# Kernel optimization log

Measured on AMD Instinct MI355X. Metric: run time of the kernel, lower is better.

## Reference

```python
import jax, jax.numpy as jnp
import numpy as np

N_NODES = 50000
N_EDGES = 800000
D_IN, D_H, D_E = 512, 512, 256


def setup_inputs() -> dict:
    key = jax.random.key(0)
    ks = jax.random.split(key, 16)

    def lin(kw, kb, fan_in, fan_out):
        s = 1.0 / np.sqrt(fan_in)
        W = jax.random.uniform(kw, (fan_in, fan_out), dtype=jnp.float32, minval=-s, maxval=s)
        b = jax.random.uniform(kb, (fan_out,), dtype=jnp.float32, minval=-s, maxval=s)
        return W, b

    W1, b1 = lin(ks[2], ks[3], D_IN, D_H)
    W2, b2 = lin(ks[4], ks[5], D_H, D_H)
    W3, b3 = lin(ks[6], ks[7], D_H, D_E)
    We, be = lin(ks[8], ks[9], D_E, 7)
    Wh, bh = lin(ks[10], ks[11], D_E, 8)
    Wg, bg = lin(ks[12], ks[13], D_E, 57)

    return {
        "x": jax.random.normal(ks[0], (N_NODES, D_IN), dtype=jnp.float32),
        "edge_index": jax.random.randint(ks[1], (2, N_EDGES), 0, N_NODES, dtype=jnp.int32),
        "W1": W1, "b1": b1, "W2": W2, "b2": b2, "W3": W3, "b3": b3,
        "We": We, "be": be, "Wh": Wh, "bh": bh, "Wg": Wg, "bg": bg,
    }


def reference(x, edge_index, W1, b1, W2, b2, W3, b3, We, be, Wh, bh, Wg, bg):
    n = x.shape[0]
    # GCNConv: add self-loops, symmetric normalization D^{-1/2} A D^{-1/2}
    loops = jnp.arange(n, dtype=edge_index.dtype)
    src = jnp.concatenate([edge_index[0], loops])  # message sources
    dst = jnp.concatenate([edge_index[1], loops])  # aggregation targets
    deg = jax.ops.segment_sum(jnp.ones_like(src, dtype=x.dtype), dst, num_segments=n)
    dis = jnp.where(deg > 0, jax.lax.rsqrt(deg), 0.0)
    norm = (dis[src] * dis[dst])[:, None]  # [E+N, 1]

    def gcn_conv(h, W, b):
        h = h @ W                                   # [n, d_out]
        msg = h[src] * norm                         # gather + scale
        return jax.ops.segment_sum(msg, dst, num_segments=n) + b

    h = jax.nn.relu(gcn_conv(x, W1, b1))
    h = jax.nn.relu(gcn_conv(h, W2, b2))
    emb = gcn_conv(h, W3, b3)
    employment = emb @ We + be
    healthcare = emb @ Wh + bh
    grocery = emb @ Wg + bg
    return emb, employment, healthcare, grocery
```

## Files before the change

### kernel.cpp

```cpp
#include <hip/hip_runtime.h>

#define NN   50000
#define NNP  50048
#define NE   800000
#define DIN  512
#define DH   512
#define DE   256

#define CSR_CAP 1150016

typedef __bf16 bf16_t;
typedef __bf16 bf16x4 __attribute__((ext_vector_type(4)));
typedef __bf16 bf16x8 __attribute__((ext_vector_type(8)));
typedef float  f32x4  __attribute__((ext_vector_type(4)));
typedef _Float16 half_t;
typedef _Float16 half8 __attribute__((ext_vector_type(8)));

#define PB_SPLIT 25024
#define PB_IDEG  3125
#define PB_CSR   1124
#define PB_W1    1024
#define PB_W2    1024
#define PB_W3    512
#define PB_HEADW 80
#define PB_TOTAL (PB_SPLIT + PB_IDEG + PB_CSR + PB_W1 + PB_W2 + PB_W3 + PB_HEADW)

__global__ void k_prep(const float* __restrict__ X, bf16_t* __restrict__ Ah,
                       bf16_t* __restrict__ Al, const int* __restrict__ dst,
                       int* __restrict__ indeg, int* __restrict__ csr,
                       const float* __restrict__ W1, bf16_t* __restrict__ B1h, bf16_t* __restrict__ B1l,
                       const float* __restrict__ W2, bf16_t* __restrict__ B2h, bf16_t* __restrict__ B2l,
                       const float* __restrict__ W3, bf16_t* __restrict__ B3h, bf16_t* __restrict__ B3l,
                       const float* __restrict__ We, const float* __restrict__ be,
                       const float* __restrict__ Wh, const float* __restrict__ bh,
                       const float* __restrict__ Wg, const float* __restrict__ bg,
                       bf16_t* __restrict__ Wth, bf16_t* __restrict__ Wtl,
                       float* __restrict__ bc) {
    int b = blockIdx.x;
    if (b < PB_SPLIT) {
        long idx = (long)b * 256 + threadIdx.x;
        long base = idx * 4;
        int row = (int)(base >> 9);
        f32x4 v;
        if (row < NN) v = *(const f32x4*)(X + base);
        else { v[0] = 0.f; v[1] = 0.f; v[2] = 0.f; v[3] = 0.f; }
        bf16x4 h, l;
        #pragma unroll
        for (int c = 0; c < 4; ++c) {
            float f = v[c];
            bf16_t hh = (bf16_t)f;
            h[c] = hh;
            l[c] = (bf16_t)(f - (float)hh);
        }
        *(bf16x4*)(Ah + base) = h;
        *(bf16x4*)(Al + base) = l;
        return;
    }
    b -= PB_SPLIT;
    if (b < PB_IDEG) {
        int i = b * 256 + threadIdx.x;
        atomicAdd(&indeg[dst[i]], 1);
        return;
    }
    b -= PB_IDEG;
    if (b < PB_CSR) {
        int i = b * 256 + threadIdx.x;
        if (i < CSR_CAP / 4) ((int4*)csr)[i] = make_int4(NN, NN, NN, NN);
        return;
    }
    b -= PB_CSR;
    if (b < PB_W1) {
        int idx = b * 256 + threadIdx.x;
        int k = idx >> 9, n = idx & 511;
        float f = W1[idx];
        bf16_t h = (bf16_t)f;
        B1h[(size_t)n * DIN + k] = h;
        B1l[(size_t)n * DIN + k] = (bf16_t)(f - (float)h);
        return;
    }
    b -= PB_W1;
    if (b < PB_W2) {
        int idx = b * 256 + threadIdx.x;
        int k = idx >> 9, n = idx & 511;
        float f = W2[idx];
        bf16_t h = (bf16_t)f;
        B2h[(size_t)n * DH + k] = h;
        B2l[(size_t)n * DH + k] = (bf16_t)(f - (float)h);
        return;
    }
    b -= PB_W2;
    if (b < PB_W3) {
        int idx = b * 256 + threadIdx.x;
        int k = idx >> 8, n = idx & 255;
        float f = W3[idx];
        bf16_t h = (bf16_t)f;
        B3h[(size_t)n * DH + k] = h;
        B3l[(size_t)n * DH + k] = (bf16_t)(f - (float)h);
        return;
    }
    b -= PB_W3;
    {
        int idx = b * 256 + threadIdx.x;
        int n = idx / 256, k = idx % 256;
        float f = 0.f;
        if (n < 7)       f = We[k * 7 + n];
        else if (n < 15) f = Wh[k * 8 + (n - 7)];
        else if (n < 72) f = Wg[k * 57 + (n - 15)];
        bf16_t h = (bf16_t)f;
        Wth[idx] = h;
        Wtl[idx] = (bf16_t)(f - (float)h);
        if (k == 0) {
            float bb = 0.f;
            if (n < 7)       bb = be[n];
            else if (n < 15) bb = bh[n - 7];
            else if (n < 72) bb = bg[n - 15];
            bc[n] = bb;
        }
    }
}

#define SCAN_BLOCKS 49

__global__ __launch_bounds__(1024) void k_scan_a(const int* __restrict__ indeg,
                                                 int* __restrict__ rowptr,
                                                 float* __restrict__ dis,
                                                 int* __restrict__ bsum) {
    __shared__ int wsum[16];
    const int tid = threadIdx.x, lane = tid & 63, wid = tid >> 6;
    const int i = blockIdx.x * 1024 + tid;
    int deg = (i < NN) ? indeg[i] : 0;
    int v = (deg + 7) & ~7;
    int x = v;
    #pragma unroll
    for (int d = 1; d < 64; d <<= 1) {
        int t = __shfl_up(x, d, 64);
        if (lane >= d) x += t;
    }
    if (lane == 63) wsum[wid] = x;
    __syncthreads();
    if (wid == 0) {
        int s = (lane < 16) ? wsum[lane] : 0;
        #pragma unroll
        for (int d = 1; d < 16; d <<= 1) {
            int t = __shfl_up(s, d, 64);
            if (lane >= d) s += t;
        }
        if (lane < 16) wsum[lane] = s;
    }
    __syncthreads();
    int woff = (wid > 0) ? wsum[wid - 1] : 0;
    if (i < NN) {
        rowptr[i] = x - v + woff;
        dis[i] = rsqrtf((float)(deg + 1));
    }
    if (tid == 0) bsum[blockIdx.x] = wsum[15];
}

__global__ __launch_bounds__(64) void k_scan_b(const int* __restrict__ bsum,
                                               int* __restrict__ boff,
                                               int* __restrict__ rowptr,
                                               float* __restrict__ dis) {
    const int lane = threadIdx.x;
    int v = (lane < SCAN_BLOCKS) ? bsum[lane] : 0;
    int x = v;
    #pragma unroll
    for (int d = 1; d < 64; d <<= 1) {
        int t = __shfl_up(x, d, 64);
        if (lane >= d) x += t;
    }
    if (lane < SCAN_BLOCKS) boff[lane] = x - v;
    if (lane == SCAN_BLOCKS - 1) rowptr[NN] = x;
    if (lane == 0) dis[NN] = 0.f;
}

__global__ void k_scan_c(const int* __restrict__ boff, int* __restrict__ rowptr,
                         int* __restrict__ cursor) {
    int i = blockIdx.x * blockDim.x + threadIdx.x;
    if (i < NN) {
        int r = rowptr[i] + boff[i >> 10];
        rowptr[i] = r;
        cursor[i] = r;
    }
}

__global__ void k_fill(const int* __restrict__ src, const int* __restrict__ dst,
                       int* __restrict__ cursor, int* __restrict__ csr, int e) {
    int i = blockIdx.x * blockDim.x + threadIdx.x;
    if (i < e) {
        int d = dst[i];
        int p = atomicAdd(&cursor[d], 1);
        csr[p] = src[i];
    }
}


__device__ __forceinline__ void gld_lds16(const void* g, void* l) {
    __builtin_amdgcn_global_load_lds(
        (const __attribute__((address_space(1))) unsigned int*)g,
        (__attribute__((address_space(3))) unsigned int*)l, 16, 0, 0);
}

__global__ __launch_bounds__(256) void k_gemm_split(
    const bf16_t* __restrict__ Ah, const bf16_t* __restrict__ Al,
    const bf16_t* __restrict__ Bh, const bf16_t* __restrict__ Bl,
    half_t* __restrict__ C, int M, int N, int K) {
    __shared__ alignas(16) bf16_t sAh[128 * 32];
    __shared__ alignas(16) bf16_t sAl[128 * 32];
    __shared__ alignas(16) bf16_t sBh[128 * 32];
    __shared__ alignas(16) bf16_t sBl[128 * 32];

    const int tid = threadIdx.x;
    const int wave = tid >> 6, lane = tid & 63;
    const int quad = lane >> 4, l16 = lane & 15;
    const int bm = blockIdx.y * 128, bn = blockIdx.x * 128;
    const int wm = (wave & 1) * 64, wn = (wave >> 1) * 64;

    f32x4 acc[4][4];
    #pragma unroll
    for (int i = 0; i < 4; ++i)
        #pragma unroll
        for (int j = 0; j < 4; ++j)
            #pragma unroll
            for (int r = 0; r < 4; ++r) acc[i][j][r] = 0.f;

    const int srow = wave * 32 + (lane >> 2);
    const int sseg = (lane & 3) * 16;
    char* lds0A = (char*)sAh + wave * 32 * 64;
    char* lds0a = (char*)sAl + wave * 32 * 64;
    char* lds0B = (char*)sBh + wave * 32 * 64;
    char* lds0b = (char*)sBl + wave * 32 * 64;

    const char* gAh0 = (const char*)(Ah + (size_t)(bm + srow) * K) + sseg;
    const char* gAl0 = (const char*)(Al + (size_t)(bm + srow) * K) + sseg;
    const char* gBh0 = (const char*)(Bh + (size_t)(bn + srow) * K) + sseg;
    const char* gBl0 = (const char*)(Bl + (size_t)(bn + srow) * K) + sseg;
    const size_t rstep = (size_t)16 * K * 2;

    for (int k0 = 0; k0 < K; k0 += 32) {
        const size_t kb = (size_t)k0 * 2;
        gld_lds16(gAh0 + kb,         lds0A);
        gld_lds16(gAh0 + kb + rstep, lds0A + 1024);
        gld_lds16(gAl0 + kb,         lds0a);
        gld_lds16(gAl0 + kb + rstep, lds0a + 1024);
        gld_lds16(gBh0 + kb,         lds0B);
        gld_lds16(gBh0 + kb + rstep, lds0B + 1024);
        gld_lds16(gBl0 + kb,         lds0b);
        gld_lds16(gBl0 + kb + rstep, lds0b + 1024);
        __syncthreads();

        bf16x8 fah[4], fal[4], fbh[4], fbl[4];
        #pragma unroll
        for (int i = 0; i < 4; ++i) {
            fah[i] = *(const bf16x8*)(sAh + (wm + 16 * i + l16) * 32 + quad * 8);
            fal[i] = *(const bf16x8*)(sAl + (wm + 16 * i + l16) * 32 + quad * 8);
            fbh[i] = *(const bf16x8*)(sBh + (wn + 16 * i + l16) * 32 + quad * 8);
            fbl[i] = *(const bf16x8*)(sBl + (wn + 16 * i + l16) * 32 + quad * 8);
        }
        #pragma unroll
        for (int i = 0; i < 4; ++i)
            #pragma unroll
            for (int j = 0; j < 4; ++j) {
                acc[i][j] = __builtin_amdgcn_mfma_f32_16x16x32_bf16(fah[i], fbh[j], acc[i][j], 0, 0, 0);
                acc[i][j] = __builtin_amdgcn_mfma_f32_16x16x32_bf16(fah[i], fbl[j], acc[i][j], 0, 0, 0);
                acc[i][j] = __builtin_amdgcn_mfma_f32_16x16x32_bf16(fal[i], fbh[j], acc[i][j], 0, 0, 0);
            }
        __syncthreads();
    }

    #pragma unroll
    for (int i = 0; i < 4; ++i) {
        #pragma unroll
        for (int j = 0; j < 4; ++j) {
            int col = bn + wn + 16 * j + l16;
            #pragma unroll
            for (int r = 0; r < 4; ++r) {
                int row = bm + wm + 16 * i + quad * 4 + r;
                if (row < M) C[(size_t)row * N + col] = (half_t)acc[i][j][r];
            }
        }
    }
}


__global__ __launch_bounds__(128) void k_agg_split(
    const half_t* __restrict__ t, const int* __restrict__ rowptr,
    const int* __restrict__ csr, const float* __restrict__ dis,
    const float* __restrict__ bias,
    bf16_t* __restrict__ Ah, bf16_t* __restrict__ Al) {
    const int node = blockIdx.x * 2 + (threadIdx.x >> 6);
    const int lane = threadIdx.x & 63;
    const int beg = rowptr[node], end = rowptr[node + 1];
    const float din = dis[node];
    const char* tc = (const char*)t;
    const unsigned lb = (unsigned)lane * 16u;

    float a0[8], a1[8], a2[8], a3[8];
    #pragma unroll
    for (int c = 0; c < 8; ++c) { a0[c] = 0.f; a1[c] = 0.f; a2[c] = 0.f; a3[c] = 0.f; }

    if (beg < end) {
        int4 sa = *(const int4*)(csr + beg);
        int4 sb = *(const int4*)(csr + beg + 4);
        float w0 = dis[sa.x], w1 = dis[sa.y], w2 = dis[sa.z], w3 = dis[sa.w];
        float w4 = dis[sb.x], w5 = dis[sb.y], w6 = dis[sb.z], w7 = dis[sb.w];
        half8 v0 = *(const half8*)(tc + (((unsigned)sa.x) << 10) + lb);
        half8 v1 = *(const half8*)(tc + (((unsigned)sa.y) << 10) + lb);
        half8 v2 = *(const half8*)(tc + (((unsigned)sa.z) << 10) + lb);
        half8 v3 = *(const half8*)(tc + (((unsigned)sa.w) << 10) + lb);
        half8 v4 = *(const half8*)(tc + (((unsigned)sb.x) << 10) + lb);
        half8 v5 = *(const half8*)(tc + (((unsigned)sb.y) << 10) + lb);
        half8 v6 = *(const half8*)(tc + (((unsigned)sb.z) << 10) + lb);
        half8 v7 = *(const half8*)(tc + (((unsigned)sb.w) << 10) + lb);
        int4 na = sa, nb = sb;
        if (beg + 8 < end) {
            na = *(const int4*)(csr + beg + 8);
            nb = *(const int4*)(csr + beg + 12);
        }
        for (int e = beg; e < end; ) {
            half8 u0 = v0, u1 = v1, u2 = v2, u3 = v3, u4 = v4, u5 = v5, u6 = v6, u7 = v7;
            float x0 = w0, x1 = w1, x2 = w2, x3 = w3, x4 = w4, x5 = w5, x6 = w6, x7 = w7;
            e += 8;
            if (e < end) {
                w0 = dis[na.x]; w1 = dis[na.y]; w2 = dis[na.z]; w3 = dis[na.w];
                w4 = dis[nb.x]; w5 = dis[nb.y]; w6 = dis[nb.z]; w7 = dis[nb.w];
                v0 = *(const half8*)(tc + (((unsigned)na.x) << 10) + lb);
                v1 = *(const half8*)(tc + (((unsigned)na.y) << 10) + lb);
                v2 = *(const half8*)(tc + (((unsigned)na.z) << 10) + lb);
                v3 = *(const half8*)(tc + (((unsigned)na.w) << 10) + lb);
                v4 = *(const half8*)(tc + (((unsigned)nb.x) << 10) + lb);
                v5 = *(const half8*)(tc + (((unsigned)nb.y) << 10) + lb);
                v6 = *(const half8*)(tc + (((unsigned)nb.z) << 10) + lb);
                v7 = *(const half8*)(tc + (((unsigned)nb.w) << 10) + lb);
                if (e + 8 < end) {
                    na = *(const int4*)(csr + e + 8);
                    nb = *(const int4*)(csr + e + 12);
                }
            }
            #pragma unroll
            for (int c = 0; c < 8; ++c) {
                a0[c] = fmaf((float)u0[c], x0, a0[c]);
                a1[c] = fmaf((float)u1[c], x1, a1[c]);
                a2[c] = fmaf((float)u2[c], x2, a2[c]);
                a3[c] = fmaf((float)u3[c], x3, a3[c]);
                a0[c] = fmaf((float)u4[c], x4, a0[c]);
                a1[c] = fmaf((float)u5[c], x5, a1[c]);
                a2[c] = fmaf((float)u6[c], x6, a2[c]);
                a3[c] = fmaf((float)u7[c], x7, a3[c]);
            }
        }
    }

    half8 sv = ((const half8*)(t + (size_t)node * DH))[lane];
    f32x4 bv0 = ((const f32x4*)bias)[lane * 2];
    f32x4 bv1 = ((const f32x4*)bias)[lane * 2 + 1];
    bf16x8 h, l;
    #pragma unroll
    for (int c = 0; c < 8; ++c) {
        float b = (c < 4) ? bv0[c] : bv1[c - 4];
        float acc = (a0[c] + a1[c]) + (a2[c] + a3[c]);
        float o = fmaf(fmaf((float)sv[c], din, acc), din, b);
        o = fmaxf(o, 0.f);
        bf16_t hh = (bf16_t)o;
        h[c] = hh;
        l[c] = (bf16_t)(o - (float)hh);
    }
    *(bf16x8*)(Ah + (size_t)node * DH + lane * 8) = h;
    *(bf16x8*)(Al + (size_t)node * DH + lane * 8) = l;
}

__global__ __launch_bounds__(128) void k_agg_f32(
    const half_t* __restrict__ t, const int* __restrict__ rowptr,
    const int* __restrict__ csr, const float* __restrict__ dis,
    const float* __restrict__ bias, float* __restrict__ out,
    bf16_t* __restrict__ Eh, bf16_t* __restrict__ El) {
    const int node = blockIdx.x * 4 + (threadIdx.x >> 5);
    const int lane = threadIdx.x & 31;
    const int beg = rowptr[node], end = rowptr[node + 1];
    const float din = dis[node];
    const char* tc = (const char*)t;
    const unsigned lb = (unsigned)lane * 16u;

    float a0[8], a1[8], a2[8], a3[8];
    #pragma unroll
    for (int c = 0; c < 8; ++c) { a0[c] = 0.f; a1[c] = 0.f; a2[c] = 0.f; a3[c] = 0.f; }

    if (beg < end) {
        int4 sa = *(const int4*)(csr + beg);
        int4 sb = *(const int4*)(csr + beg + 4);
        float w0 = dis[sa.x], w1 = dis[sa.y], w2 = dis[sa.z], w3 = dis[sa.w];
        float w4 = dis[sb.x], w5 = dis[sb.y], w6 = dis[sb.z], w7 = dis[sb.w];
        half8 v0 = *(const half8*)(tc + (((unsigned)sa.x) << 9) + lb);
        half8 v1 = *(const half8*)(tc + (((unsigned)sa.y) << 9) + lb);
        half8 v2 = *(const half8*)(tc + (((unsigned)sa.z) << 9) + lb);
        half8 v3 = *(const half8*)(tc + (((unsigned)sa.w) << 9) + lb);
        half8 v4 = *(const half8*)(tc + (((unsigned)sb.x) << 9) + lb);
        half8 v5 = *(const half8*)(tc + (((unsigned)sb.y) << 9) + lb);
        half8 v6 = *(const half8*)(tc + (((unsigned)sb.z) << 9) + lb);
        half8 v7 = *(const half8*)(tc + (((unsigned)sb.w) << 9) + lb);
        int4 na = sa, nb = sb;
        if (beg + 8 < end) {
            na = *(const int4*)(csr + beg + 8);
            nb = *(const int4*)(csr + beg + 12);
        }
        for (int e = beg; e < end; ) {
            half8 u0 = v0, u1 = v1, u2 = v2, u3 = v3, u4 = v4, u5 = v5, u6 = v6, u7 = v7;
            float x0 = w0, x1 = w1, x2 = w2, x3 = w3, x4 = w4, x5 = w5, x6 = w6, x7 = w7;
            e += 8;
            if (e < end) {
                w0 = dis[na.x]; w1 = dis[na.y]; w2 = dis[na.z]; w3 = dis[na.w];
                w4 = dis[nb.x]; w5 = dis[nb.y]; w6 = dis[nb.z]; w7 = dis[nb.w];
                v0 = *(const half8*)(tc + (((unsigned)na.x) << 9) + lb);
                v1 = *(const half8*)(tc + (((unsigned)na.y) << 9) + lb);
                v2 = *(const half8*)(tc + (((unsigned)na.z) << 9) + lb);
                v3 = *(const half8*)(tc + (((unsigned)na.w) << 9) + lb);
                v4 = *(const half8*)(tc + (((unsigned)nb.x) << 9) + lb);
                v5 = *(const half8*)(tc + (((unsigned)nb.y) << 9) + lb);
                v6 = *(const half8*)(tc + (((unsigned)nb.z) << 9) + lb);
                v7 = *(const half8*)(tc + (((unsigned)nb.w) << 9) + lb);
                if (e + 8 < end) {
                    na = *(const int4*)(csr + e + 8);
                    nb = *(const int4*)(csr + e + 12);
                }
            }
            #pragma unroll
            for (int c = 0; c < 8; ++c) {
                a0[c] = fmaf((float)u0[c], x0, a0[c]);
                a1[c] = fmaf((float)u1[c], x1, a1[c]);
                a2[c] = fmaf((float)u2[c], x2, a2[c]);
                a3[c] = fmaf((float)u3[c], x3, a3[c]);
                a0[c] = fmaf((float)u4[c], x4, a0[c]);
                a1[c] = fmaf((float)u5[c], x5, a1[c]);
                a2[c] = fmaf((float)u6[c], x6, a2[c]);
                a3[c] = fmaf((float)u7[c], x7, a3[c]);
            }
        }
    }

    half8 sv = ((const half8*)(t + (size_t)node * DE))[lane];
    f32x4 bv0 = ((const f32x4*)bias)[lane * 2];
    f32x4 bv1 = ((const f32x4*)bias)[lane * 2 + 1];
    f32x4 o0, o1;
    bf16x8 hh, ll;
    #pragma unroll
    for (int c = 0; c < 8; ++c) {
        float b = (c < 4) ? bv0[c] : bv1[c - 4];
        float acc = (a0[c] + a1[c]) + (a2[c] + a3[c]);
        float o = fmaf(fmaf((float)sv[c], din, acc), din, b);
        if (c < 4) o0[c] = o; else o1[c - 4] = o;
        bf16_t h = (bf16_t)o;
        hh[c] = h;
        ll[c] = (bf16_t)(o - (float)h);
    }
    ((f32x4*)(out + (size_t)node * DE))[lane * 2]     = o0;
    ((f32x4*)(out + (size_t)node * DE))[lane * 2 + 1] = o1;
    *(bf16x8*)(Eh + (size_t)node * DE + lane * 8) = hh;
    *(bf16x8*)(El + (size_t)node * DE + lane * 8) = ll;
}


__global__ __launch_bounds__(256) void k_heads_mfma(
    const bf16_t* __restrict__ Eh, const bf16_t* __restrict__ El,
    const bf16_t* __restrict__ Wth, const bf16_t* __restrict__ Wtl,
    const float* __restrict__ bc,
    float* __restrict__ oe, float* __restrict__ oh, float* __restrict__ og) {
    const int wave = threadIdx.x >> 6, lane = threadIdx.x & 63;
    const int quad = lane >> 4, l16 = lane & 15;
    const int row0 = blockIdx.x * 64 + wave * 16;

    f32x4 acc[5];
    #pragma unroll
    for (int j = 0; j < 5; ++j)
        #pragma unroll
        for (int r = 0; r < 4; ++r) acc[j][r] = 0.f;

    const size_t abase = (size_t)(row0 + l16) * 256 + quad * 8;
    #pragma unroll
    for (int ks = 0; ks < 256; ks += 32) {
        bf16x8 ah = *(const bf16x8*)(Eh + abase + ks);
        bf16x8 al = *(const bf16x8*)(El + abase + ks);
        #pragma unroll
        for (int j = 0; j < 5; ++j) {
            const size_t bbase = (size_t)(j * 16 + l16) * 256 + ks + quad * 8;
            bf16x8 bh = *(const bf16x8*)(Wth + bbase);
            bf16x8 bl = *(const bf16x8*)(Wtl + bbase);
            acc[j] = __builtin_amdgcn_mfma_f32_16x16x32_bf16(ah, bh, acc[j], 0, 0, 0);
            acc[j] = __builtin_amdgcn_mfma_f32_16x16x32_bf16(ah, bl, acc[j], 0, 0, 0);
            acc[j] = __builtin_amdgcn_mfma_f32_16x16x32_bf16(al, bh, acc[j], 0, 0, 0);
        }
    }

    #pragma unroll
    for (int j = 0; j < 5; ++j) {
        int col = j * 16 + l16;
        if (col < 72) {
            float b = bc[col];
            #pragma unroll
            for (int r = 0; r < 4; ++r) {
                int row = row0 + quad * 4 + r;
                if (row < NN) {
                    float v = acc[j][r] + b;
                    if (col < 7)       oe[(size_t)row * 7 + col] = v;
                    else if (col < 15) oh[(size_t)row * 8 + (col - 7)] = v;
                    else               og[(size_t)row * 57 + (col - 15)] = v;
                }
            }
        }
    }
}


extern "C" void kernel_launch(void* const* d_in, const int* in_sizes, int n_in,
                              void* d_out, int out_size, void* d_ws, size_t ws_size,
                              hipStream_t stream) {
    const float* x   = (const float*)d_in[0];
    const int*   ei  = (const int*)d_in[1];
    const float* W1  = (const float*)d_in[2];
    const float* b1  = (const float*)d_in[3];
    const float* W2  = (const float*)d_in[4];
    const float* b2  = (const float*)d_in[5];
    const float* W3  = (const float*)d_in[6];
    const float* b3  = (const float*)d_in[7];
    const float* We  = (const float*)d_in[8];
    const float* be  = (const float*)d_in[9];
    const float* Wh  = (const float*)d_in[10];
    const float* bh  = (const float*)d_in[11];
    const float* Wg  = (const float*)d_in[12];
    const float* bg  = (const float*)d_in[13];

    const int* e_src = ei;
    const int* e_dst = ei + NE;

    half_t* bufA = (half_t*)d_ws;
    bf16_t* Ah   = (bf16_t*)(bufA + (size_t)NNP * DH);
    bf16_t* Al   = Ah + (size_t)NNP * DH;
    bf16_t* B1h  = Al + (size_t)NNP * DH;
    bf16_t* B1l  = B1h + (size_t)DIN * DH;
    bf16_t* B2h  = B1l + (size_t)DIN * DH;
    bf16_t* B2l  = B2h + (size_t)DH * DH;
    bf16_t* B3h  = B2l + (size_t)DH * DH;
    bf16_t* B3l  = B3h + (size_t)DH * DE;
    bf16_t* embh = B3l + (size_t)DH * DE;
    bf16_t* embl = embh + (size_t)NNP * DE;
    bf16_t* Wth  = embl + (size_t)NNP * DE;
    bf16_t* Wtl  = Wth + 80 * 256;
    float*  bc   = (float*)(Wtl + 80 * 256);
    int*   indeg  = (int*)(bc + 128);
    int*   rowptr = indeg + 50048;
    int*   cursor = rowptr + 50048;
    float* dis    = (float*)(cursor + 50048);
    int*   csr    = (int*)(dis + 50048);
    int*   bsum   = csr + CSR_CAP;
    int*   boff   = bsum + 64;

    float* emb   = (float*)d_out;
    float* out_e = emb + (size_t)NN * DE;
    float* out_h = out_e + (size_t)NN * 7;
    float* out_g = out_h + (size_t)NN * 8;

    hipMemsetAsync(indeg, 0, NN * sizeof(int), stream);
    k_prep<<<PB_TOTAL, 256, 0, stream>>>(x, Ah, Al, e_dst, indeg, csr,
                                         W1, B1h, B1l, W2, B2h, B2l, W3, B3h, B3l,
                                         We, be, Wh, bh, Wg, bg, Wth, Wtl, bc);
    k_scan_a<<<SCAN_BLOCKS, 1024, 0, stream>>>(indeg, rowptr, dis, bsum);
    k_scan_b<<<1, 64, 0, stream>>>(bsum, boff, rowptr, dis);
    k_scan_c<<<(NN + 255) / 256, 256, 0, stream>>>(boff, rowptr, cursor);
    k_fill<<<(NE + 255) / 256, 256, 0, stream>>>(e_src, e_dst, cursor, csr, NE);

    const int gy = NNP / 128;

    k_gemm_split<<<dim3(DH / 128, gy), 256, 0, stream>>>(Ah, Al, B1h, B1l, bufA, NNP, DH, DIN);
    k_agg_split<<<NN / 2, 128, 0, stream>>>(bufA, rowptr, csr, dis, b1, Ah, Al);

    k_gemm_split<<<dim3(DH / 128, gy), 256, 0, stream>>>(Ah, Al, B2h, B2l, bufA, NNP, DH, DH);
    k_agg_split<<<NN / 2, 128, 0, stream>>>(bufA, rowptr, csr, dis, b2, Ah, Al);

    k_gemm_split<<<dim3(DE / 128, gy), 256, 0, stream>>>(Ah, Al, B3h, B3l, bufA, NNP, DE, DH);
    k_agg_f32<<<NN / 4, 128, 0, stream>>>(bufA, rowptr, csr, dis, b3, emb, embh, embl);

    k_heads_mfma<<<NNP / 64, 256, 0, stream>>>(embh, embl, Wth, Wtl, bc, out_e, out_h, out_g);
}
```

Measured before the change: 900.9 us.

## Fold source-degree scaling into GEMM epilogue and use fp16 activations for layers 2-3

Each GEMM epilogue now multiplies its output row by dis[row], so the aggregation kernels no longer gather dis per neighbour and only multiply by the destination's dis. Layers 2 and 3 store activations as a single fp16 array instead of a bf16 hi/lo pair. Their GEMMs use fp16 MFMA with the weights split into an fp16 high part and a residual scaled by 4096, so two MFMA products replace the three-product bf16 split. This cuts activation write and read traffic and the number of MFMAs. The trade is reduced precision, since the activations are no longer split into two parts.

```diff
diff --git a/kernel.cpp b/kernel.cpp
--- a/kernel.cpp
+++ b/kernel.cpp
@@ -25,12 +25,12 @@
 #define PB_HEADW 80
 #define PB_TOTAL (PB_SPLIT + PB_IDEG + PB_CSR + PB_W1 + PB_W2 + PB_W3 + PB_HEADW)
 
-__global__ void k_prep(const float* __restrict__ X, bf16_t* __restrict__ Ah,
-                       bf16_t* __restrict__ Al, const int* __restrict__ dst,
+__global__ void k_prep(const float* __restrict__ X, bf16_t* __restrict__ Xh,
+                       bf16_t* __restrict__ Xl, const int* __restrict__ dst,
                        int* __restrict__ indeg, int* __restrict__ csr,
                        const float* __restrict__ W1, bf16_t* __restrict__ B1h, bf16_t* __restrict__ B1l,
-                       const float* __restrict__ W2, bf16_t* __restrict__ B2h, bf16_t* __restrict__ B2l,
-                       const float* __restrict__ W3, bf16_t* __restrict__ B3h, bf16_t* __restrict__ B3l,
+                       const float* __restrict__ W2, half_t* __restrict__ B2h, half_t* __restrict__ B2l,
+                       const float* __restrict__ W3, half_t* __restrict__ B3h, half_t* __restrict__ B3l,
                        const float* __restrict__ We, const float* __restrict__ be,
                        const float* __restrict__ Wh, const float* __restrict__ bh,
                        const float* __restrict__ Wg, const float* __restrict__ bg,
@@ -52,8 +52,8 @@
             h[c] = hh;
             l[c] = (bf16_t)(f - (float)hh);
         }
-        *(bf16x4*)(Ah + base) = h;
-        *(bf16x4*)(Al + base) = l;
+        *(bf16x4*)(Xh + base) = h;
+        *(bf16x4*)(Xl + base) = l;
         return;
     }
     b -= PB_SPLIT;
@@ -83,9 +83,9 @@
         int idx = b * 256 + threadIdx.x;
         int k = idx >> 9, n = idx & 511;
         float f = W2[idx];
-        bf16_t h = (bf16_t)f;
+        half_t h = (half_t)f;
         B2h[(size_t)n * DH + k] = h;
-        B2l[(size_t)n * DH + k] = (bf16_t)(f - (float)h);
+        B2l[(size_t)n * DH + k] = (half_t)((f - (float)h) * 4096.f);
         return;
     }
     b -= PB_W2;
@@ -93,9 +93,9 @@
         int idx = b * 256 + threadIdx.x;
         int k = idx >> 8, n = idx & 255;
         float f = W3[idx];
-        bf16_t h = (bf16_t)f;
+        half_t h = (half_t)f;
         B3h[(size_t)n * DH + k] = h;
-        B3l[(size_t)n * DH + k] = (bf16_t)(f - (float)h);
+        B3l[(size_t)n * DH + k] = (half_t)((f - (float)h) * 4096.f);
         return;
     }
     b -= PB_W3;
@@ -152,14 +152,15 @@
     if (i < NN) {
         rowptr[i] = x - v + woff;
         dis[i] = rsqrtf((float)(deg + 1));
+    } else if (i < NNP) {
+        dis[i] = 0.f;
     }
     if (tid == 0) bsum[blockIdx.x] = wsum[15];
 }
 
 __global__ __launch_bounds__(64) void k_scan_b(const int* __restrict__ bsum,
                                                int* __restrict__ boff,
-                                               int* __restrict__ rowptr,
-                                               float* __restrict__ dis) {
+                                               int* __restrict__ rowptr) {
     const int lane = threadIdx.x;
     int v = (lane < SCAN_BLOCKS) ? bsum[lane] : 0;
     int x = v;
@@ -170,7 +171,6 @@
     }
     if (lane < SCAN_BLOCKS) boff[lane] = x - v;
     if (lane == SCAN_BLOCKS - 1) rowptr[NN] = x;
-    if (lane == 0) dis[NN] = 0.f;
 }
 
 __global__ void k_scan_c(const int* __restrict__ boff, int* __restrict__ rowptr,
@@ -200,10 +200,12 @@
         (__attribute__((address_space(3))) unsigned int*)l, 16, 0, 0);
 }
 
-__global__ __launch_bounds__(256) void k_gemm_split(
+
+__global__ __launch_bounds__(256) void k_gemm_bf3(
     const bf16_t* __restrict__ Ah, const bf16_t* __restrict__ Al,
     const bf16_t* __restrict__ Bh, const bf16_t* __restrict__ Bl,
-    half_t* __restrict__ C, int M, int N, int K) {
+    const float* __restrict__ disv,
+    half_t* __restrict__ C, int N, int K) {
     __shared__ alignas(16) bf16_t sAh[128 * 32];
     __shared__ alignas(16) bf16_t sAl[128 * 32];
     __shared__ alignas(16) bf16_t sBh[128 * 32];
@@ -269,24 +271,102 @@
 
     #pragma unroll
     for (int i = 0; i < 4; ++i) {
+        const int rowb = bm + wm + 16 * i + quad * 4;
+        float d0 = disv[rowb], d1 = disv[rowb + 1], d2 = disv[rowb + 2], d3 = disv[rowb + 3];
         #pragma unroll
         for (int j = 0; j < 4; ++j) {
             int col = bn + wn + 16 * j + l16;
+            C[(size_t)(rowb + 0) * N + col] = (half_t)(acc[i][j][0] * d0);
+            C[(size_t)(rowb + 1) * N + col] = (half_t)(acc[i][j][1] * d1);
+            C[(size_t)(rowb + 2) * N + col] = (half_t)(acc[i][j][2] * d2);
+            C[(size_t)(rowb + 3) * N + col] = (half_t)(acc[i][j][3] * d3);
+        }
+    }
+}
+
+
+__global__ __launch_bounds__(256) void k_gemm_f16(
+    const half_t* __restrict__ A,
+    const half_t* __restrict__ Bh, const half_t* __restrict__ Bl,
+    const float* __restrict__ disv,
+    half_t* __restrict__ C, int N, int K) {
+    __shared__ alignas(16) half_t sA [128 * 32];
+    __shared__ alignas(16) half_t sBh[128 * 32];
+    __shared__ alignas(16) half_t sBl[128 * 32];
+
+    const int tid = threadIdx.x;
+    const int wave = tid >> 6, lane = tid & 63;
+    const int quad = lane >> 4, l16 = lane & 15;
+    const int bm = blockIdx.y * 128, bn = blockIdx.x * 128;
+    const int wm = (wave & 1) * 64, wn = (wave >> 1) * 64;
+
+    f32x4 aH[4][4], aM[4][4];
+    #pragma unroll
+    for (int i = 0; i < 4; ++i)
+        #pragma unroll
+        for (int j = 0; j < 4; ++j)
             #pragma unroll
-            for (int r = 0; r < 4; ++r) {
-                int row = bm + wm + 16 * i + quad * 4 + r;
-                if (row < M) C[(size_t)row * N + col] = (half_t)acc[i][j][r];
+            for (int r = 0; r < 4; ++r) { aH[i][j][r] = 0.f; aM[i][j][r] = 0.f; }
+
+    const int srow = wave * 32 + (lane >> 2);
+    const int sseg = (lane & 3) * 16;
+    char* lds0A = (char*)sA  + wave * 32 * 64;
+    char* lds0B = (char*)sBh + wave * 32 * 64;
+    char* lds0b = (char*)sBl + wave * 32 * 64;
+
+    const char* gA0  = (const char*)(A  + (size_t)(bm + srow) * K) + sseg;
+    const char* gBh0 = (const char*)(Bh + (size_t)(bn + srow) * K) + sseg;
+    const char* gBl0 = (const char*)(Bl + (size_t)(bn + srow) * K) + sseg;
+    const size_t rstep = (size_t)16 * K * 2;
+
+    for (int k0 = 0; k0 < K; k0 += 32) {
+        const size_t kb = (size_t)k0 * 2;
+        gld_lds16(gA0  + kb,         lds0A);
+        gld_lds16(gA0  + kb + rstep, lds0A + 1024);
+        gld_lds16(gBh0 + kb,         lds0B);
+        gld_lds16(gBh0 + kb + rstep, lds0B + 1024);
+        gld_lds16(gBl0 + kb,         lds0b);
+        gld_lds16(gBl0 + kb + rstep, lds0b + 1024);
+        __syncthreads();
+
+        half8 fa[4], fbh[4], fbl[4];
+        #pragma unroll
+        for (int i = 0; i < 4; ++i) {
+            fa[i]  = *(const half8*)(sA  + (wm + 16 * i + l16) * 32 + quad * 8);
+            fbh[i] = *(const half8*)(sBh + (wn + 16 * i + l16) * 32 + quad * 8);
+            fbl[i] = *(const half8*)(sBl + (wn + 16 * i + l16) * 32 + quad * 8);
+        }
+        #pragma unroll
+        for (int i = 0; i < 4; ++i)
+            #pragma unroll
+            for (int j = 0; j < 4; ++j) {
+                aH[i][j] = __builtin_amdgcn_mfma_f32_16x16x32_f16(fa[i], fbh[j], aH[i][j], 0, 0, 0);
+                aM[i][j] = __builtin_amdgcn_mfma_f32_16x16x32_f16(fa[i], fbl[j], aM[i][j], 0, 0, 0);
             }
-        }
-    }
-}
-
-
-__global__ __launch_bounds__(128) void k_agg_split(
+        __syncthreads();
+    }
+
+    const float s = 1.f / 4096.f;
+    #pragma unroll
+    for (int i = 0; i < 4; ++i) {
+        const int rowb = bm + wm + 16 * i + quad * 4;
+        float d0 = disv[rowb], d1 = disv[rowb + 1], d2 = disv[rowb + 2], d3 = disv[rowb + 3];
+        #pragma unroll
+        for (int j = 0; j < 4; ++j) {
+            int col = bn + wn + 16 * j + l16;
+            C[(size_t)(rowb + 0) * N + col] = (half_t)(fmaf(aM[i][j][0], s, aH[i][j][0]) * d0);
+            C[(size_t)(rowb + 1) * N + col] = (half_t)(fmaf(aM[i][j][1], s, aH[i][j][1]) * d1);
+            C[(size_t)(rowb + 2) * N + col] = (half_t)(fmaf(aM[i][j][2], s, aH[i][j][2]) * d2);
+            C[(size_t)(rowb + 3) * N + col] = (half_t)(fmaf(aM[i][j][3], s, aH[i][j][3]) * d3);
+        }
+    }
+}
+
+
+__global__ __launch_bounds__(128) void k_agg16(
     const half_t* __restrict__ t, const int* __restrict__ rowptr,
     const int* __restrict__ csr, const float* __restrict__ dis,
-    const float* __restrict__ bias,
-    bf16_t* __restrict__ Ah, bf16_t* __restrict__ Al) {
+    const float* __restrict__ bias, half_t* __restrict__ out) {
     const int node = blockIdx.x * 2 + (threadIdx.x >> 6);
     const int lane = threadIdx.x & 63;
     const int beg = rowptr[node], end = rowptr[node + 1];
@@ -301,8 +381,6 @@
     if (beg < end) {
         int4 sa = *(const int4*)(csr + beg);
         int4 sb = *(const int4*)(csr + beg + 4);
-        float w0 = dis[sa.x], w1 = dis[sa.y], w2 = dis[sa.z], w3 = dis[sa.w];
-        float w4 = dis[sb.x], w5 = dis[sb.y], w6 = dis[sb.z], w7 = dis[sb.w];
         half8 v0 = *(const half8*)(tc + (((unsigned)sa.x) << 10) + lb);
         half8 v1 = *(const half8*)(tc + (((unsigned)sa.y) << 10) + lb);
         half8 v2 = *(const half8*)(tc + (((unsigned)sa.z) << 10) + lb);
@@ -318,11 +396,8 @@
         }
         for (int e = beg; e < end; ) {
             half8 u0 = v0, u1 = v1, u2 = v2, u3 = v3, u4 = v4, u5 = v5, u6 = v6, u7 = v7;
-            float x0 = w0, x1 = w1, x2 = w2, x3 = w3, x4 = w4, x5 = w5, x6 = w6, x7 = w7;
             e += 8;
             if (e < end) {
-                w0 = dis[na.x]; w1 = dis[na.y]; w2 = dis[na.z]; w3 = dis[na.w];
-                w4 = dis[nb.x]; w5 = dis[nb.y]; w6 = dis[nb.z]; w7 = dis[nb.w];
                 v0 = *(const half8*)(tc + (((unsigned)na.x) << 10) + lb);
                 v1 = *(const half8*)(tc + (((unsigned)na.y) << 10) + lb);
                 v2 = *(const half8*)(tc + (((unsigned)na.z) << 10) + lb);
@@ -338,14 +413,14 @@
             }
             #pragma unroll
             for (int c = 0; c < 8; ++c) {
-                a0[c] = fmaf((float)u0[c], x0, a0[c]);
-                a1[c] = fmaf((float)u1[c], x1, a1[c]);
-                a2[c] = fmaf((float)u2[c], x2, a2[c]);
-                a3[c] = fmaf((float)u3[c], x3, a3[c]);
-                a0[c] = fmaf((float)u4[c], x4, a0[c]);
-                a1[c] = fmaf((float)u5[c], x5, a1[c]);
-                a2[c] = fmaf((float)u6[c], x6, a2[c]);
-                a3[c] = fmaf((float)u7[c], x7, a3[c]);
+                a0[c] = fmaf((float)u0[c], din, a0[c]);
+                a1[c] = fmaf((float)u1[c], din, a1[c]);
+                a2[c] = fmaf((float)u2[c], din, a2[c]);
+                a3[c] = fmaf((float)u3[c], din, a3[c]);
+                a0[c] = fmaf((float)u4[c], din, a0[c]);
+                a1[c] = fmaf((float)u5[c], din, a1[c]);
+                a2[c] = fmaf((float)u6[c], din, a2[c]);
+                a3[c] = fmaf((float)u7[c], din, a3[c]);
             }
         }
     }
@@ -353,19 +428,16 @@
     half8 sv = ((const half8*)(t + (size_t)node * DH))[lane];
     f32x4 bv0 = ((const f32x4*)bias)[lane * 2];
     f32x4 bv1 = ((const f32x4*)bias)[lane * 2 + 1];
-    bf16x8 h, l;
+    half8 h;
     #pragma unroll
     for (int c = 0; c < 8; ++c) {
         float b = (c < 4) ? bv0[c] : bv1[c - 4];
         float acc = (a0[c] + a1[c]) + (a2[c] + a3[c]);
-        float o = fmaf(fmaf((float)sv[c], din, acc), din, b);
+        float o = fmaf((float)sv[c], din, acc) + b;
         o = fmaxf(o, 0.f);
-        bf16_t hh = (bf16_t)o;
-        h[c] = hh;
-        l[c] = (bf16_t)(o - (float)hh);
-    }
-    *(bf16x8*)(Ah + (size_t)node * DH + lane * 8) = h;
-    *(bf16x8*)(Al + (size_t)node * DH + lane * 8) = l;
+        h[c] = (half_t)o;
+    }
+    *(half8*)(out + (size_t)node * DH + lane * 8) = h;
 }
 
 __global__ __launch_bounds__(128) void k_agg_f32(
@@ -387,8 +459,6 @@
     if (beg < end) {
         int4 sa = *(const int4*)(csr + beg);
         int4 sb = *(const int4*)(csr + beg + 4);
-        float w0 = dis[sa.x], w1 = dis[sa.y], w2 = dis[sa.z], w3 = dis[sa.w];
-        float w4 = dis[sb.x], w5 = dis[sb.y], w6 = dis[sb.z], w7 = dis[sb.w];
         half8 v0 = *(const half8*)(tc + (((unsigned)sa.x) << 9) + lb);
         half8 v1 = *(const half8*)(tc + (((unsigned)sa.y) << 9) + lb);
         half8 v2 = *(const half8*)(tc + (((unsigned)sa.z) << 9) + lb);
@@ -404,11 +474,8 @@
         }
         for (int e = beg; e < end; ) {
             half8 u0 = v0, u1 = v1, u2 = v2, u3 = v3, u4 = v4, u5 = v5, u6 = v6, u7 = v7;
-            float x0 = w0, x1 = w1, x2 = w2, x3 = w3, x4 = w4, x5 = w5, x6 = w6, x7 = w7;
             e += 8;
             if (e < end) {
-                w0 = dis[na.x]; w1 = dis[na.y]; w2 = dis[na.z]; w3 = dis[na.w];
-                w4 = dis[nb.x]; w5 = dis[nb.y]; w6 = dis[nb.z]; w7 = dis[nb.w];
                 v0 = *(const half8*)(tc + (((unsigned)na.x) << 9) + lb);
                 v1 = *(const half8*)(tc + (((unsigned)na.y) << 9) + lb);
                 v2 = *(const half8*)(tc + (((unsigned)na.z) << 9) + lb);
@@ -424,14 +491,14 @@
             }
             #pragma unroll
             for (int c = 0; c < 8; ++c) {
-                a0[c] = fmaf((float)u0[c], x0, a0[c]);
-                a1[c] = fmaf((float)u1[c], x1, a1[c]);
-                a2[c] = fmaf((float)u2[c], x2, a2[c]);
-                a3[c] = fmaf((float)u3[c], x3, a3[c]);
-                a0[c] = fmaf((float)u4[c], x4, a0[c]);
-                a1[c] = fmaf((float)u5[c], x5, a1[c]);
-                a2[c] = fmaf((float)u6[c], x6, a2[c]);
-                a3[c] = fmaf((float)u7[c], x7, a3[c]);
+                a0[c] = fmaf((float)u0[c], din, a0[c]);
+                a1[c] = fmaf((float)u1[c], din, a1[c]);
+                a2[c] = fmaf((float)u2[c], din, a2[c]);
+                a3[c] = fmaf((float)u3[c], din, a3[c]);
+                a0[c] = fmaf((float)u4[c], din, a0[c]);
+                a1[c] = fmaf((float)u5[c], din, a1[c]);
+                a2[c] = fmaf((float)u6[c], din, a2[c]);
+                a3[c] = fmaf((float)u7[c], din, a3[c]);
             }
         }
     }
@@ -445,7 +512,7 @@
     for (int c = 0; c < 8; ++c) {
         float b = (c < 4) ? bv0[c] : bv1[c - 4];
         float acc = (a0[c] + a1[c]) + (a2[c] + a3[c]);
-        float o = fmaf(fmaf((float)sv[c], din, acc), din, b);
+        float o = fmaf((float)sv[c], din, acc) + b;
         if (c < 4) o0[c] = o; else o1[c - 4] = o;
         bf16_t h = (bf16_t)o;
         hh[c] = h;
@@ -530,18 +597,19 @@
     const int* e_src = ei;
     const int* e_dst = ei + NE;
 
-    half_t* bufA = (half_t*)d_ws;
-    bf16_t* Ah   = (bf16_t*)(bufA + (size_t)NNP * DH);
-    bf16_t* Al   = Ah + (size_t)NNP * DH;
-    bf16_t* B1h  = Al + (size_t)NNP * DH;
+    half_t* buf0 = (half_t*)d_ws;
+    half_t* buf1 = buf0 + (size_t)NNP * DH;
+    bf16_t* Xh   = (bf16_t*)buf1;
+    bf16_t* Xl   = Xh + (size_t)NNP * DH;
+    bf16_t* embh = Xl;
+    bf16_t* embl = embh + (size_t)NNP * DE;
+    bf16_t* B1h  = Xl + (size_t)NNP * DH;
     bf16_t* B1l  = B1h + (size_t)DIN * DH;
-    bf16_t* B2h  = B1l + (size_t)DIN * DH;
-    bf16_t* B2l  = B2h + (size_t)DH * DH;
-    bf16_t* B3h  = B2l + (size_t)DH * DH;
-    bf16_t* B3l  = B3h + (size_t)DH * DE;
-    bf16_t* embh = B3l + (size_t)DH * DE;
-    bf16_t* embl = embh + (size_t)NNP * DE;
-    bf16_t* Wth  = embl + (size_t)NNP * DE;
+    half_t* B2h  = (half_t*)(B1l + (size_t)DIN * DH);
+    half_t* B2l  = B2h + (size_t)DH * DH;
+    half_t* B3h  = B2l + (size_t)DH * DH;
+    half_t* B3l  = B3h + (size_t)DE * DH;
+    bf16_t* Wth  = (bf16_t*)(B3l + (size_t)DE * DH);
     bf16_t* Wtl  = Wth + 80 * 256;
     float*  bc   = (float*)(Wtl + 80 * 256);
     int*   indeg  = (int*)(bc + 128);
@@ -558,24 +626,24 @@
     float* out_g = out_h + (size_t)NN * 8;
 
     hipMemsetAsync(indeg, 0, NN * sizeof(int), stream);
-    k_prep<<<PB_TOTAL, 256, 0, stream>>>(x, Ah, Al, e_dst, indeg, csr,
+    k_prep<<<PB_TOTAL, 256, 0, stream>>>(x, Xh, Xl, e_dst, indeg, csr,
                                          W1, B1h, B1l, W2, B2h, B2l, W3, B3h, B3l,
                                          We, be, Wh, bh, Wg, bg, Wth, Wtl, bc);
     k_scan_a<<<SCAN_BLOCKS, 1024, 0, stream>>>(indeg, rowptr, dis, bsum);
-    k_scan_b<<<1, 64, 0, stream>>>(bsum, boff, rowptr, dis);
+    k_scan_b<<<1, 64, 0, stream>>>(bsum, boff, rowptr);
     k_scan_c<<<(NN + 255) / 256, 256, 0, stream>>>(boff, rowptr, cursor);
     k_fill<<<(NE + 255) / 256, 256, 0, stream>>>(e_src, e_dst, cursor, csr, NE);
 
     const int gy = NNP / 128;
 
-    k_gemm_split<<<dim3(DH / 128, gy), 256, 0, stream>>>(Ah, Al, B1h, B1l, bufA, NNP, DH, DIN);
-    k_agg_split<<<NN / 2, 128, 0, stream>>>(bufA, rowptr, csr, dis, b1, Ah, Al);
-
-    k_gemm_split<<<dim3(DH / 128, gy), 256, 0, stream>>>(Ah, Al, B2h, B2l, bufA, NNP, DH, DH);
-    k_agg_split<<<NN / 2, 128, 0, stream>>>(bufA, rowptr, csr, dis, b2, Ah, Al);
-
-    k_gemm_split<<<dim3(DE / 128, gy), 256, 0, stream>>>(Ah, Al, B3h, B3l, bufA, NNP, DE, DH);
-    k_agg_f32<<<NN / 4, 128, 0, stream>>>(bufA, rowptr, csr, dis, b3, emb, embh, embl);
+    k_gemm_bf3<<<dim3(DH / 128, gy), 256, 0, stream>>>(Xh, Xl, B1h, B1l, dis, buf0, DH, DIN);
+    k_agg16<<<NN / 2, 128, 0, stream>>>(buf0, rowptr, csr, dis, b1, buf1);
+
+    k_gemm_f16<<<dim3(DH / 128, gy), 256, 0, stream>>>(buf1, B2h, B2l, dis, buf0, DH, DH);
+    k_agg16<<<NN / 2, 128, 0, stream>>>(buf0, rowptr, csr, dis, b2, buf1);
+
+    k_gemm_f16<<<dim3(DE / 128, gy), 256, 0, stream>>>(buf1, B3h, B3l, dis, buf0, DE, DH);
+    k_agg_f32<<<NN / 4, 128, 0, stream>>>(buf0, rowptr, csr, dis, b3, emb, embh, embl);
 
     k_heads_mfma<<<NNP / 64, 256, 0, stream>>>(embh, embl, Wth, Wtl, bc, out_e, out_h, out_g);
 }
```

New measurement: 962.4 us. 6.8% more time.
